# Performance work log

Measured on AMD Instinct MI355X. Metric: run time of the kernel, lower is better.

The kernel has to match this reference:

```python
import jax, jax.numpy as jnp
import numpy as np
from jax import lax

VOCAB, EMBED, HID, MID = 32000, 200, 10, 5
BSZ, SEQ = 256, 512
LN_EPS = 1e-5


def setup_inputs() -> dict:
    key = jax.random.key(0)
    ks = jax.random.split(key, 10)
    s = 0.1
    return {
        "src_tokens": jax.random.randint(ks[0], (BSZ, SEQ), 0, VOCAB, dtype=jnp.int64)
        if jax.config.jax_enable_x64 else jax.random.randint(ks[0], (BSZ, SEQ), 0, VOCAB, dtype=jnp.int32),
        "h0": jax.random.normal(ks[1], (1, BSZ, HID), jnp.float32),
        "c0": jax.random.normal(ks[2], (1, BSZ, HID), jnp.float32),
        "embed_W": jax.random.normal(ks[3], (VOCAB, EMBED), jnp.float32),
        "W_ih": jax.random.normal(ks[4], (4 * HID, EMBED), jnp.float32) * s,
        "W_hh": jax.random.normal(ks[5], (4 * HID, HID), jnp.float32) * s,
        "b_ih": jax.random.normal(ks[6], (4 * HID,), jnp.float32) * s,
        "b_hh": jax.random.normal(ks[7], (4 * HID,), jnp.float32) * s,
        "W1": jax.random.normal(ks[8], (MID, HID), jnp.float32) * s,
        "b1": jnp.zeros((MID,), jnp.float32),
        "ln_g": jnp.ones((MID,), jnp.float32),
        "ln_b": jnp.zeros((MID,), jnp.float32),
        "W2": jax.random.normal(ks[9], (1, MID), jnp.float32) * s,
        "b2": jnp.zeros((1,), jnp.float32),
    }


def reference(src_tokens, h0, c0, embed_W, W_ih, W_hh, b_ih, b_hh,
              W1, b1, ln_g, ln_b, W2, b2):
    # Embedding lookup -> [B, S, E] -> time-major [S, B, E]
    x = embed_W[src_tokens].astype(jnp.float32)
    x = jnp.transpose(x, (1, 0, 2))
    # Precompute input contribution to all 4 gates (i,f,g,o order, as torch)
    gates_x = jnp.einsum('sbe,ge->sbg', x, W_ih) + b_ih + b_hh  # [S, B, 4H]

    def step(carry, gx):
        h, c = carry
        gates = gx + h @ W_hh.T
        i, f, g, o = jnp.split(gates, 4, axis=-1)
        i = jax.nn.sigmoid(i)
        f = jax.nn.sigmoid(f)
        g = jnp.tanh(g)
        o = jax.nn.sigmoid(o)
        c = f * c + i * g
        h = o * jnp.tanh(c)
        return (h, c), None

    (hn, _), _ = lax.scan(step, (h0[0], c0[0]), gates_x)  # hn: [B, H]

    z = hn @ W1.T + b1  # [B, 5]
    mu = jnp.mean(z, axis=-1, keepdims=True)
    var = jnp.mean(jnp.square(z - mu), axis=-1, keepdims=True)
    z = (z - mu) * lax.rsqrt(var + LN_EPS) * ln_g + ln_b
    out = jax.nn.sigmoid(z @ W2.T + b2)  # [B, 1]
    return out[:, 0]  # squeeze -> [B]
```

## Files before the change

kernel.cpp:

```cpp
#include <hip/hip_runtime.h>
#include <math.h>

#define VOCAB 32000
#define EMBED 200
#define HID   10
#define GATES 40
#define BSZ   256
#define SEQ   512
#define PF    8

#define RPB    64
#define EPITCH 202
#define WROW   48

__device__ __forceinline__ float rcp_fast(float x) { return __builtin_amdgcn_rcpf(x); }
__device__ __forceinline__ float exp2_fast(float x) { return __builtin_amdgcn_exp2f(x); }
__device__ __forceinline__ float readlane_f(float v, int l) {
    return __int_as_float(__builtin_amdgcn_readlane(__float_as_int(v), l));
}
template <int Q>
__device__ __forceinline__ float quad_bcast(float v) {
    return __int_as_float(__builtin_amdgcn_mov_dpp(
        __float_as_int(v), Q * 0x55, 0xF, 0xF, true));
}

#define SC_SIG (-1.442695041f)
#define SC_TNH (-2.885390082f)

__global__ __launch_bounds__(256, 1) void proj_kernel(
    const float* __restrict__ embed, const float* __restrict__ Wih,
    const float* __restrict__ bih,   const float* __restrict__ bhh,
    float* __restrict__ proj)
{
    __shared__ float eT[RPB * EPITCH];
    __shared__ float wT[EMBED * WROW];

    const int tid = threadIdx.x;
    const int v0  = blockIdx.x * RPB;

    for (int idx = tid; idx < GATES * EMBED; idx += 256) {
        int g = idx / EMBED, k = idx - g * EMBED;
        wT[k * WROW + (g / 10) * 12 + (g % 10)] = Wih[idx];
    }
    {
        const float4* src = (const float4*)(embed + (size_t)v0 * EMBED);
        for (int f = tid; f < RPB * 50; f += 256) {
            float4 x = src[f];
            int r = f / 50, c = f - r * 50;
            float* dst = &eT[r * EPITCH + c * 4];
            dst[0] = x.x; dst[1] = x.y; dst[2] = x.z; dst[3] = x.w;
        }
    }
    __syncthreads();

    const int tr = tid & 63;
    const int tg = tid >> 6;

    float acc[10];
    #pragma unroll
    for (int i = 0; i < 10; ++i) acc[i] = 0.f;

    for (int k0 = 0; k0 < EMBED; k0 += 8) {
        float2 e01 = *(const float2*)&eT[tr * EPITCH + k0];
        float2 e23 = *(const float2*)&eT[tr * EPITCH + k0 + 2];
        float2 e45 = *(const float2*)&eT[tr * EPITCH + k0 + 4];
        float2 e67 = *(const float2*)&eT[tr * EPITCH + k0 + 6];
        float e[8] = {e01.x, e01.y, e23.x, e23.y, e45.x, e45.y, e67.x, e67.y};
        #pragma unroll
        for (int kk = 0; kk < 8; ++kk) {
            const float* wr = &wT[(k0 + kk) * WROW + tg * 12];
            float4 wa = *(const float4*)(wr);
            float4 wb = *(const float4*)(wr + 4);
            float2 wc = *(const float2*)(wr + 8);
            acc[0] = fmaf(e[kk], wa.x, acc[0]);
            acc[1] = fmaf(e[kk], wa.y, acc[1]);
            acc[2] = fmaf(e[kk], wa.z, acc[2]);
            acc[3] = fmaf(e[kk], wa.w, acc[3]);
            acc[4] = fmaf(e[kk], wb.x, acc[4]);
            acc[5] = fmaf(e[kk], wb.y, acc[5]);
            acc[6] = fmaf(e[kk], wb.z, acc[6]);
            acc[7] = fmaf(e[kk], wb.w, acc[7]);
            acc[8] = fmaf(e[kk], wc.x, acc[8]);
            acc[9] = fmaf(e[kk], wc.y, acc[9]);
        }
    }

    const float sc = (tg == 2) ? SC_TNH : SC_SIG;
    const int gbase = tg * 10;
    float* op = &proj[(size_t)(v0 + tr) * GATES + gbase];
    #pragma unroll
    for (int i = 0; i < 5; ++i) {
        float2 o;
        o.x = (acc[2*i]   + bih[gbase + 2*i]   + bhh[gbase + 2*i])   * sc;
        o.y = (acc[2*i+1] + bih[gbase + 2*i+1] + bhh[gbase + 2*i+1]) * sc;
        *(float2*)(op + 2 * i) = o;
    }
}

__global__ __launch_bounds__(64, 1) void lstm_rec(
    const int*   __restrict__ tok,  const float* __restrict__ proj,
    const float* __restrict__ h0,   const float* __restrict__ c0,
    const float* __restrict__ Whh,
    const float* __restrict__ W1,   const float* __restrict__ b1,
    const float* __restrict__ lng,  const float* __restrict__ lnb,
    const float* __restrict__ W2,   const float* __restrict__ b2,
    float* __restrict__ out)
{
    __shared__ int tok_s[SEQ + 2 * PF];

    const int b    = blockIdx.x;
    const int lane = threadIdx.x;
    const int j0   = min(lane >> 2, HID - 1);
    const int k4   = lane & 3;
    const int gate = k4 * HID + j0;

    #pragma unroll
    for (int k = 0; k < SEQ / 64; ++k)
        tok_s[k * 64 + lane] = tok[b * SEQ + k * 64 + lane];
    if (lane < 2 * PF) tok_s[SEQ + lane] = 0;
    __syncthreads();

    const float am  = (k4 == 2) ? 2.f : 1.f;
    const float amc = 1.f - am;
    const float amn = (k4 == 2) ? SC_TNH : SC_SIG;

    float w[HID];
    #pragma unroll
    for (int j = 0; j < HID; ++j) w[j] = amn * Whh[gate * HID + j];

    float hs[HID];
    #pragma unroll
    for (int u = 0; u < HID; ++u) hs[u] = h0[b * HID + u];
    float c_own = c0[b * HID + j0];

    int   tk_cur[PF], tk_nxt[PF];
    float gx_cur[PF], gx_nxt[PF];
    #pragma unroll
    for (int k = 0; k < PF; ++k) tk_cur[k] = tok_s[k];
    #pragma unroll
    for (int k = 0; k < PF; ++k) gx_cur[k] = proj[tk_cur[k] * GATES + gate];
    #pragma unroll
    for (int k = 0; k < PF; ++k) tk_nxt[k] = tok_s[PF + k];

    for (int s0 = 0; s0 < SEQ; s0 += PF) {
        #pragma unroll
        for (int k = 0; k < PF; ++k)
            gx_nxt[k] = proj[tk_nxt[k] * GATES + gate];
        #pragma unroll
        for (int k = 0; k < PF; ++k)
            tk_cur[k] = tok_s[s0 + 2 * PF + k];

        #pragma unroll
        for (int k = 0; k < PF; ++k) {
            float a0 = gx_cur[k], a1 = 0.f, a2 = 0.f, a3 = 0.f;
            a0 = fmaf(hs[0], w[0], a0); a1 = fmaf(hs[1], w[1], a1);
            a2 = fmaf(hs[2], w[2], a2); a3 = fmaf(hs[3], w[3], a3);
            a0 = fmaf(hs[4], w[4], a0); a1 = fmaf(hs[5], w[5], a1);
            a2 = fmaf(hs[6], w[6], a2); a3 = fmaf(hs[7], w[7], a3);
            a0 = fmaf(hs[8], w[8], a0); a1 = fmaf(hs[9], w[9], a1);
            float dt = (a0 + a2) + (a1 + a3);

            float t   = exp2_fast(dt);
            float sg  = rcp_fast(1.f + t);
            float val = fmaf(am, sg, amc);

            float iv = quad_bcast<0>(val);
            float fv = quad_bcast<1>(val);
            float gv = quad_bcast<2>(val);
            float ov = quad_bcast<3>(val);

            c_own = fmaf(fv, c_own, iv * gv);
            float t2 = exp2_fast(c_own * SC_TNH);
            float th = fmaf(2.f, rcp_fast(1.f + t2), -1.f);
            float h_own = ov * th;

            hs[0] = readlane_f(h_own, 0);  hs[1] = readlane_f(h_own, 4);
            hs[2] = readlane_f(h_own, 8);  hs[3] = readlane_f(h_own, 12);
            hs[4] = readlane_f(h_own, 16); hs[5] = readlane_f(h_own, 20);
            hs[6] = readlane_f(h_own, 24); hs[7] = readlane_f(h_own, 28);
            hs[8] = readlane_f(h_own, 32); hs[9] = readlane_f(h_own, 36);
        }

        #pragma unroll
        for (int k = 0; k < PF; ++k) {
            gx_cur[k] = gx_nxt[k];
            tk_nxt[k] = tk_cur[k];
        }
    }

    if (lane == 0) {
        float z[5];
        float mu = 0.f;
        #pragma unroll
        for (int m = 0; m < 5; ++m) {
            float a = b1[m];
            #pragma unroll
            for (int j = 0; j < HID; ++j) a = fmaf(hs[j], W1[m * HID + j], a);
            z[m] = a; mu += a;
        }
        mu *= 0.2f;
        float var = 0.f;
        #pragma unroll
        for (int m = 0; m < 5; ++m) { float d = z[m] - mu; var = fmaf(d, d, var); }
        var *= 0.2f;
        float rs = rsqrtf(var + 1e-5f);
        float acc = b2[0];
        #pragma unroll
        for (int m = 0; m < 5; ++m) {
            float zn = fmaf((z[m] - mu) * rs, lng[m], lnb[m]);
            acc = fmaf(zn, W2[m], acc);
        }
        out[b] = 1.f / (1.f + __expf(-acc));
    }
}

extern "C" void kernel_launch(void* const* d_in, const int* in_sizes, int n_in,
                              void* d_out, int out_size, void* d_ws, size_t ws_size,
                              hipStream_t stream) {
    const int*   tok   = (const int*)  d_in[0];
    const float* h0    = (const float*)d_in[1];
    const float* c0    = (const float*)d_in[2];
    const float* embed = (const float*)d_in[3];
    const float* Wih   = (const float*)d_in[4];
    const float* Whh   = (const float*)d_in[5];
    const float* bih   = (const float*)d_in[6];
    const float* bhh   = (const float*)d_in[7];
    const float* W1    = (const float*)d_in[8];
    const float* b1    = (const float*)d_in[9];
    const float* lng   = (const float*)d_in[10];
    const float* lnb   = (const float*)d_in[11];
    const float* W2    = (const float*)d_in[12];
    const float* b2    = (const float*)d_in[13];
    float* out  = (float*)d_out;
    float* proj = (float*)d_ws;

    hipLaunchKernelGGL(proj_kernel, dim3(VOCAB / RPB), dim3(256), 0, stream,
                       embed, Wih, bih, bhh, proj);
    hipLaunchKernelGGL(lstm_rec, dim3(BSZ), dim3(64), 0, stream,
                       tok, proj, h0, c0, Whh, W1, b1, lng, lnb, W2, b2, out);
}
```

Before: 99.02 us.

## Process two batch sequences per wavefront to interleave independent LSTM recurrences

Each 64-lane block now runs two batch elements' LSTM recurrences in lockstep, interleaving their FMA, transcendental, DPP and readlane chains so one chain's latency can hide behind the other's. The grid is halved to 128 blocks, and the token prefetch becomes a simpler one-chunk-ahead scheme. The goal is to hide latency on the serial per-step dependency chain. The costs are lower occupancy (128 waves across 256 CUs) and more register pressure.

```diff
diff --git a/kernel.cpp b/kernel.cpp
--- a/kernel.cpp
+++ b/kernel.cpp
@@ -106,18 +106,21 @@
     const float* __restrict__ W2,   const float* __restrict__ b2,
     float* __restrict__ out)
 {
-    __shared__ int tok_s[SEQ + 2 * PF];
-
-    const int b    = blockIdx.x;
+    __shared__ int tok_s[2][SEQ + PF];
+
+    const int bb   = blockIdx.x;
+    const int bA   = 2 * bb, bB = 2 * bb + 1;
     const int lane = threadIdx.x;
     const int j0   = min(lane >> 2, HID - 1);
     const int k4   = lane & 3;
     const int gate = k4 * HID + j0;
 
     #pragma unroll
-    for (int k = 0; k < SEQ / 64; ++k)
-        tok_s[k * 64 + lane] = tok[b * SEQ + k * 64 + lane];
-    if (lane < 2 * PF) tok_s[SEQ + lane] = 0;
+    for (int k = 0; k < SEQ / 64; ++k) {
+        tok_s[0][k * 64 + lane] = tok[bA * SEQ + k * 64 + lane];
+        tok_s[1][k * 64 + lane] = tok[bB * SEQ + k * 64 + lane];
+    }
+    if (lane < PF) { tok_s[0][SEQ + lane] = 0; tok_s[1][SEQ + lane] = 0; }
     __syncthreads();
 
     const float am  = (k4 == 2) ? 2.f : 1.f;
@@ -128,89 +131,102 @@
     #pragma unroll
     for (int j = 0; j < HID; ++j) w[j] = amn * Whh[gate * HID + j];
 
-    float hs[HID];
-    #pragma unroll
-    for (int u = 0; u < HID; ++u) hs[u] = h0[b * HID + u];
-    float c_own = c0[b * HID + j0];
-
-    int   tk_cur[PF], tk_nxt[PF];
-    float gx_cur[PF], gx_nxt[PF];
-    #pragma unroll
-    for (int k = 0; k < PF; ++k) tk_cur[k] = tok_s[k];
-    #pragma unroll
-    for (int k = 0; k < PF; ++k) gx_cur[k] = proj[tk_cur[k] * GATES + gate];
-    #pragma unroll
-    for (int k = 0; k < PF; ++k) tk_nxt[k] = tok_s[PF + k];
+    float hsA[HID], hsB[HID];
+    #pragma unroll
+    for (int u = 0; u < HID; ++u) { hsA[u] = h0[bA * HID + u]; hsB[u] = h0[bB * HID + u]; }
+    float cA = c0[bA * HID + j0];
+    float cB = c0[bB * HID + j0];
+
+    float gxA[PF], gxB[PF], gxAn[PF], gxBn[PF];
+    #pragma unroll
+    for (int k = 0; k < PF; ++k) {
+        gxA[k] = proj[tok_s[0][k] * GATES + gate];
+        gxB[k] = proj[tok_s[1][k] * GATES + gate];
+    }
 
     for (int s0 = 0; s0 < SEQ; s0 += PF) {
         #pragma unroll
-        for (int k = 0; k < PF; ++k)
-            gx_nxt[k] = proj[tk_nxt[k] * GATES + gate];
-        #pragma unroll
-        for (int k = 0; k < PF; ++k)
-            tk_cur[k] = tok_s[s0 + 2 * PF + k];
-
-        #pragma unroll
         for (int k = 0; k < PF; ++k) {
-            float a0 = gx_cur[k], a1 = 0.f, a2 = 0.f, a3 = 0.f;
-            a0 = fmaf(hs[0], w[0], a0); a1 = fmaf(hs[1], w[1], a1);
-            a2 = fmaf(hs[2], w[2], a2); a3 = fmaf(hs[3], w[3], a3);
-            a0 = fmaf(hs[4], w[4], a0); a1 = fmaf(hs[5], w[5], a1);
-            a2 = fmaf(hs[6], w[6], a2); a3 = fmaf(hs[7], w[7], a3);
-            a0 = fmaf(hs[8], w[8], a0); a1 = fmaf(hs[9], w[9], a1);
-            float dt = (a0 + a2) + (a1 + a3);
-
-            float t   = exp2_fast(dt);
-            float sg  = rcp_fast(1.f + t);
-            float val = fmaf(am, sg, amc);
-
-            float iv = quad_bcast<0>(val);
-            float fv = quad_bcast<1>(val);
-            float gv = quad_bcast<2>(val);
-            float ov = quad_bcast<3>(val);
-
-            c_own = fmaf(fv, c_own, iv * gv);
-            float t2 = exp2_fast(c_own * SC_TNH);
-            float th = fmaf(2.f, rcp_fast(1.f + t2), -1.f);
-            float h_own = ov * th;
-
-            hs[0] = readlane_f(h_own, 0);  hs[1] = readlane_f(h_own, 4);
-            hs[2] = readlane_f(h_own, 8);  hs[3] = readlane_f(h_own, 12);
-            hs[4] = readlane_f(h_own, 16); hs[5] = readlane_f(h_own, 20);
-            hs[6] = readlane_f(h_own, 24); hs[7] = readlane_f(h_own, 28);
-            hs[8] = readlane_f(h_own, 32); hs[9] = readlane_f(h_own, 36);
+            gxAn[k] = proj[tok_s[0][s0 + PF + k] * GATES + gate];
+            gxBn[k] = proj[tok_s[1][s0 + PF + k] * GATES + gate];
         }
 
         #pragma unroll
         for (int k = 0; k < PF; ++k) {
-            gx_cur[k] = gx_nxt[k];
-            tk_nxt[k] = tk_cur[k];
-        }
+            float a0 = gxA[k], a1 = 0.f, a2 = 0.f, a3 = 0.f;
+            float q0 = gxB[k], q1 = 0.f, q2 = 0.f, q3 = 0.f;
+            a0 = fmaf(hsA[0], w[0], a0); q0 = fmaf(hsB[0], w[0], q0);
+            a1 = fmaf(hsA[1], w[1], a1); q1 = fmaf(hsB[1], w[1], q1);
+            a2 = fmaf(hsA[2], w[2], a2); q2 = fmaf(hsB[2], w[2], q2);
+            a3 = fmaf(hsA[3], w[3], a3); q3 = fmaf(hsB[3], w[3], q3);
+            a0 = fmaf(hsA[4], w[4], a0); q0 = fmaf(hsB[4], w[4], q0);
+            a1 = fmaf(hsA[5], w[5], a1); q1 = fmaf(hsB[5], w[5], q1);
+            a2 = fmaf(hsA[6], w[6], a2); q2 = fmaf(hsB[6], w[6], q2);
+            a3 = fmaf(hsA[7], w[7], a3); q3 = fmaf(hsB[7], w[7], q3);
+            a0 = fmaf(hsA[8], w[8], a0); q0 = fmaf(hsB[8], w[8], q0);
+            a1 = fmaf(hsA[9], w[9], a1); q1 = fmaf(hsB[9], w[9], q1);
+            float dtA = (a0 + a2) + (a1 + a3);
+            float dtB = (q0 + q2) + (q1 + q3);
+
+            float tA  = exp2_fast(dtA);      float tB  = exp2_fast(dtB);
+            float sgA = rcp_fast(1.f + tA);  float sgB = rcp_fast(1.f + tB);
+            float vA  = fmaf(am, sgA, amc);  float vB  = fmaf(am, sgB, amc);
+
+            float ivA = quad_bcast<0>(vA);   float ivB = quad_bcast<0>(vB);
+            float fvA = quad_bcast<1>(vA);   float fvB = quad_bcast<1>(vB);
+            float gvA = quad_bcast<2>(vA);   float gvB = quad_bcast<2>(vB);
+            float ovA = quad_bcast<3>(vA);   float ovB = quad_bcast<3>(vB);
+
+            cA = fmaf(fvA, cA, ivA * gvA);   cB = fmaf(fvB, cB, ivB * gvB);
+            float t2A = exp2_fast(cA * SC_TNH);
+            float t2B = exp2_fast(cB * SC_TNH);
+            float thA = fmaf(2.f, rcp_fast(1.f + t2A), -1.f);
+            float thB = fmaf(2.f, rcp_fast(1.f + t2B), -1.f);
+            float hA  = ovA * thA;           float hB  = ovB * thB;
+
+            hsA[0] = readlane_f(hA, 0);  hsB[0] = readlane_f(hB, 0);
+            hsA[1] = readlane_f(hA, 4);  hsB[1] = readlane_f(hB, 4);
+            hsA[2] = readlane_f(hA, 8);  hsB[2] = readlane_f(hB, 8);
+            hsA[3] = readlane_f(hA, 12); hsB[3] = readlane_f(hB, 12);
+            hsA[4] = readlane_f(hA, 16); hsB[4] = readlane_f(hB, 16);
+            hsA[5] = readlane_f(hA, 20); hsB[5] = readlane_f(hB, 20);
+            hsA[6] = readlane_f(hA, 24); hsB[6] = readlane_f(hB, 24);
+            hsA[7] = readlane_f(hA, 28); hsB[7] = readlane_f(hB, 28);
+            hsA[8] = readlane_f(hA, 32); hsB[8] = readlane_f(hB, 32);
+            hsA[9] = readlane_f(hA, 36); hsB[9] = readlane_f(hB, 36);
+        }
+
+        #pragma unroll
+        for (int k = 0; k < PF; ++k) { gxA[k] = gxAn[k]; gxB[k] = gxBn[k]; }
     }
 
     if (lane == 0) {
-        float z[5];
-        float mu = 0.f;
-        #pragma unroll
-        for (int m = 0; m < 5; ++m) {
-            float a = b1[m];
+        #pragma unroll
+        for (int which = 0; which < 2; ++which) {
+            const float* hv = which ? hsB : hsA;
+            float z[5];
+            float mu = 0.f;
             #pragma unroll
-            for (int j = 0; j < HID; ++j) a = fmaf(hs[j], W1[m * HID + j], a);
-            z[m] = a; mu += a;
-        }
-        mu *= 0.2f;
-        float var = 0.f;
-        #pragma unroll
-        for (int m = 0; m < 5; ++m) { float d = z[m] - mu; var = fmaf(d, d, var); }
-        var *= 0.2f;
-        float rs = rsqrtf(var + 1e-5f);
-        float acc = b2[0];
-        #pragma unroll
-        for (int m = 0; m < 5; ++m) {
-            float zn = fmaf((z[m] - mu) * rs, lng[m], lnb[m]);
-            acc = fmaf(zn, W2[m], acc);
-        }
-        out[b] = 1.f / (1.f + __expf(-acc));
+            for (int m = 0; m < 5; ++m) {
+                float a = b1[m];
+                #pragma unroll
+                for (int j = 0; j < HID; ++j) a = fmaf(hv[j], W1[m * HID + j], a);
+                z[m] = a; mu += a;
+            }
+            mu *= 0.2f;
+            float var = 0.f;
+            #pragma unroll
+            for (int m = 0; m < 5; ++m) { float d = z[m] - mu; var = fmaf(d, d, var); }
+            var *= 0.2f;
+            float rs = rsqrtf(var + 1e-5f);
+            float acc = b2[0];
+            #pragma unroll
+            for (int m = 0; m < 5; ++m) {
+                float zn = fmaf((z[m] - mu) * rs, lng[m], lnb[m]);
+                acc = fmaf(zn, W2[m], acc);
+            }
+            out[which ? bB : bA] = 1.f / (1.f + __expf(-acc));
+        }
     }
 }
 
@@ -236,6 +252,6 @@
 
     hipLaunchKernelGGL(proj_kernel, dim3(VOCAB / RPB), dim3(256), 0, stream,
                        embed, Wih, bih, bhh, proj);
-    hipLaunchKernelGGL(lstm_rec, dim3(BSZ), dim3(64), 0, stream,
+    hipLaunchKernelGGL(lstm_rec, dim3(BSZ / 2), dim3(64), 0, stream,
                        tok, proj, h0, c0, Whh, W1, b1, lng, lnb, W2, b2, out);
 }
```

Result: slower. 127.3 us (+28.6%).

## Restructure vocab projection to split-K with shuffle reduction and direct global loads

Applied to the files above, without the earlier changes.

The vocab-wide projection kernel no longer stages embedding rows in shared memory. Each group of 8 threads now owns one row, and each thread loads a slice of the embedding dimension straight from global memory with float4 loads and accumulates all 40 gates. Partial sums are combined with xor shuffles before the output is written. This removes the embedding LDS staging, shrinks shared memory, and launches twice as many blocks for better occupancy, at the cost of 40 accumulators per thread, more weight reads from LDS per FMA, and shuffle reductions.

```diff
diff --git a/kernel.cpp b/kernel.cpp
--- a/kernel.cpp
+++ b/kernel.cpp
@@ -9,9 +9,7 @@
 #define SEQ   512
 #define PF    8
 
-#define RPB    64
-#define EPITCH 202
-#define WROW   48
+#define WROW3 44
 
 __device__ __forceinline__ float rcp_fast(float x) { return __builtin_amdgcn_rcpf(x); }
 __device__ __forceinline__ float exp2_fast(float x) { return __builtin_amdgcn_exp2f(x); }
@@ -27,73 +25,71 @@
 #define SC_SIG (-1.442695041f)
 #define SC_TNH (-2.885390082f)
 
-__global__ __launch_bounds__(256, 1) void proj_kernel(
+__global__ __launch_bounds__(256) void proj_kernel(
     const float* __restrict__ embed, const float* __restrict__ Wih,
     const float* __restrict__ bih,   const float* __restrict__ bhh,
     float* __restrict__ proj)
 {
-    __shared__ float eT[RPB * EPITCH];
-    __shared__ float wT[EMBED * WROW];
-
+    __shared__ float wT[EMBED * WROW3];
     const int tid = threadIdx.x;
-    const int v0  = blockIdx.x * RPB;
 
     for (int idx = tid; idx < GATES * EMBED; idx += 256) {
         int g = idx / EMBED, k = idx - g * EMBED;
-        wT[k * WROW + (g / 10) * 12 + (g % 10)] = Wih[idx];
+        wT[k * WROW3 + g] = Wih[idx];
+    }
+    __syncthreads();
+
+    const int r  = blockIdx.x * 32 + (tid >> 3);
+    const int li = tid & 7;
+    const float* er = embed + (size_t)r * EMBED;
+
+    float acc[GATES];
+    #pragma unroll
+    for (int g = 0; g < GATES; ++g) acc[g] = 0.f;
+
+#define FMA40(K, EV) do {                                                   \
+    const float* wr_ = &wT[(K) * WROW3];                                    \
+    _Pragma("unroll")                                                       \
+    for (int q = 0; q < 10; ++q) {                                          \
+        float4 wv = *(const float4*)(wr_ + q * 4);                          \
+        acc[4*q+0] = fmaf((EV), wv.x, acc[4*q+0]);                          \
+        acc[4*q+1] = fmaf((EV), wv.y, acc[4*q+1]);                          \
+        acc[4*q+2] = fmaf((EV), wv.z, acc[4*q+2]);                          \
+        acc[4*q+3] = fmaf((EV), wv.w, acc[4*q+3]);                          \
+    }                                                                       \
+} while (0)
+
+    #pragma unroll
+    for (int c = 0; c < 6; ++c) {
+        const int k0 = c * 32 + li * 4;
+        float4 e = *(const float4*)(er + k0);
+        FMA40(k0 + 0, e.x);
+        FMA40(k0 + 1, e.y);
+        FMA40(k0 + 2, e.z);
+        FMA40(k0 + 3, e.w);
     }
     {
-        const float4* src = (const float4*)(embed + (size_t)v0 * EMBED);
-        for (int f = tid; f < RPB * 50; f += 256) {
-            float4 x = src[f];
-            int r = f / 50, c = f - r * 50;
-            float* dst = &eT[r * EPITCH + c * 4];
-            dst[0] = x.x; dst[1] = x.y; dst[2] = x.z; dst[3] = x.w;
-        }
-    }
-    __syncthreads();
-
-    const int tr = tid & 63;
-    const int tg = tid >> 6;
-
-    float acc[10];
-    #pragma unroll
-    for (int i = 0; i < 10; ++i) acc[i] = 0.f;
-
-    for (int k0 = 0; k0 < EMBED; k0 += 8) {
-        float2 e01 = *(const float2*)&eT[tr * EPITCH + k0];
-        float2 e23 = *(const float2*)&eT[tr * EPITCH + k0 + 2];
-        float2 e45 = *(const float2*)&eT[tr * EPITCH + k0 + 4];
-        float2 e67 = *(const float2*)&eT[tr * EPITCH + k0 + 6];
-        float e[8] = {e01.x, e01.y, e23.x, e23.y, e45.x, e45.y, e67.x, e67.y};
-        #pragma unroll
-        for (int kk = 0; kk < 8; ++kk) {
-            const float* wr = &wT[(k0 + kk) * WROW + tg * 12];
-            float4 wa = *(const float4*)(wr);
-            float4 wb = *(const float4*)(wr + 4);
-            float2 wc = *(const float2*)(wr + 8);
-            acc[0] = fmaf(e[kk], wa.x, acc[0]);
-            acc[1] = fmaf(e[kk], wa.y, acc[1]);
-            acc[2] = fmaf(e[kk], wa.z, acc[2]);
-            acc[3] = fmaf(e[kk], wa.w, acc[3]);
-            acc[4] = fmaf(e[kk], wb.x, acc[4]);
-            acc[5] = fmaf(e[kk], wb.y, acc[5]);
-            acc[6] = fmaf(e[kk], wb.z, acc[6]);
-            acc[7] = fmaf(e[kk], wb.w, acc[7]);
-            acc[8] = fmaf(e[kk], wc.x, acc[8]);
-            acc[9] = fmaf(e[kk], wc.y, acc[9]);
-        }
-    }
-
-    const float sc = (tg == 2) ? SC_TNH : SC_SIG;
-    const int gbase = tg * 10;
-    float* op = &proj[(size_t)(v0 + tr) * GATES + gbase];
-    #pragma unroll
-    for (int i = 0; i < 5; ++i) {
-        float2 o;
-        o.x = (acc[2*i]   + bih[gbase + 2*i]   + bhh[gbase + 2*i])   * sc;
-        o.y = (acc[2*i+1] + bih[gbase + 2*i+1] + bhh[gbase + 2*i+1]) * sc;
-        *(float2*)(op + 2 * i) = o;
+        const int k0 = 192 + li;
+        float e = er[k0];
+        FMA40(k0, e);
+    }
+#undef FMA40
+
+    #pragma unroll
+    for (int g = 0; g < GATES; ++g) {
+        float v = acc[g];
+        v += __shfl_xor(v, 1, 64);
+        v += __shfl_xor(v, 2, 64);
+        v += __shfl_xor(v, 4, 64);
+        acc[g] = v;
+    }
+
+    const int g0 = li * 5;
+    #pragma unroll
+    for (int j = 0; j < 5; ++j) {
+        int g = g0 + j;
+        float sc = (g >= 20 && g < 30) ? SC_TNH : SC_SIG;
+        proj[(size_t)r * GATES + g] = (acc[g] + bih[g] + bhh[g]) * sc;
     }
 }
 
@@ -234,7 +230,7 @@
     float* out  = (float*)d_out;
     float* proj = (float*)d_ws;
 
-    hipLaunchKernelGGL(proj_kernel, dim3(VOCAB / RPB), dim3(256), 0, stream,
+    hipLaunchKernelGGL(proj_kernel, dim3(VOCAB / 32), dim3(256), 0, stream,
                        embed, Wih, bih, bhh, proj);
     hipLaunchKernelGGL(lstm_rec, dim3(BSZ), dim3(64), 0, stream,
                        tok, proj, h0, c0, Whh, W1, b1, lng, lnb, W2, b2, out);
```

Measured after the change: 98.41 us. Within noise of the previous version (-0.6%).
